# Kernel optimization log

Measured on AMD Instinct MI355X. Metric: run time of the kernel, lower is better.

## Reference

```python
import jax, jax.numpy as jnp
import numpy as np

D_MODEL = 1024
D_FF = 4096
NUM_EXPERTS = 8
TOP_K = 2


def setup_inputs() -> dict:
    key = jax.random.key(0)
    ks = jax.random.split(key, 9)
    s_in = 1.0 / np.sqrt(D_MODEL)
    s_ff = 1.0 / np.sqrt(D_FF)
    return {
        "x": jax.random.normal(ks[0], (2, 1024, D_MODEL), dtype=jnp.float32),
        "Wg": jax.random.uniform(ks[1], (D_MODEL, NUM_EXPERTS), minval=-s_in, maxval=s_in, dtype=jnp.float32),
        "bg": jax.random.uniform(ks[2], (NUM_EXPERTS,), minval=-s_in, maxval=s_in, dtype=jnp.float32),
        "W1": jax.random.uniform(ks[3], (NUM_EXPERTS, D_MODEL, D_FF), minval=-s_in, maxval=s_in, dtype=jnp.float32),
        "b1": jax.random.uniform(ks[4], (NUM_EXPERTS, D_FF), minval=-s_in, maxval=s_in, dtype=jnp.float32),
        "W2": jax.random.uniform(ks[5], (NUM_EXPERTS, D_MODEL, D_FF), minval=-s_in, maxval=s_in, dtype=jnp.float32),
        "b2": jax.random.uniform(ks[6], (NUM_EXPERTS, D_FF), minval=-s_in, maxval=s_in, dtype=jnp.float32),
        "W3": jax.random.uniform(ks[7], (NUM_EXPERTS, D_FF, D_MODEL), minval=-s_ff, maxval=s_ff, dtype=jnp.float32),
        "b3": jax.random.uniform(ks[8], (NUM_EXPERTS, D_MODEL), minval=-s_ff, maxval=s_ff, dtype=jnp.float32),
    }


def reference(x, Wg, bg, W1, b1, W2, b2, W3, b3):
    B, S, D = x.shape
    xf = x.reshape(-1, D)                                   # [N, D]
    N = xf.shape[0]

    # ---- Router (eval mode: no noise) ----
    logits = xf @ Wg + bg                                   # [N, E]
    top_logits, top_idx = jax.lax.top_k(logits, TOP_K)      # [N, K]
    top_w = jax.nn.softmax(top_logits, axis=-1)             # softmax over the top-k logits
    # scatter top-k weights into dense [N, E]; indices are unique per row
    comb_w = jnp.zeros_like(logits).at[jnp.arange(N)[:, None], top_idx].set(top_w)

    # ---- Experts: GLU-MLP, dense per-expert (weights are 0 for unrouted tokens) ----
    h1 = jnp.einsum('nd,edf->enf', xf, W1) + b1[:, None, :]  # [E, N, F]
    h2 = jnp.einsum('nd,edf->enf', xf, W2) + b2[:, None, :]
    hidden = jax.nn.gelu(h1, approximate=False) * h2         # torch nn.GELU is exact (erf)
    expert_out = jnp.einsum('enf,efd->end', hidden, W3) + b3[:, None, :]  # [E, N, D]

    # ---- Weighted combine ----
    final = jnp.einsum('end,ne->nd', expert_out, comb_w)     # [N, D]
    aux_loss = 0.0  # eval mode: aux loss inactive
    return final.reshape(B, S, D), aux_loss
```

## Files before the change

### kernel.cpp

```cpp
#include <hip/hip_runtime.h>
#include <hip/hip_bf16.h>
#include <math.h>

#define D_MODEL 1024
#define D_FF    4096
#define NE      8
#define MT      256

typedef __bf16 bf16x8 __attribute__((ext_vector_type(8)));
typedef float  f32x4  __attribute__((ext_vector_type(4)));

__device__ __forceinline__ void async16(const void* g, void* l) {
    __builtin_amdgcn_global_load_lds(
        (__attribute__((address_space(1))) uint32_t*)g,
        (__attribute__((address_space(3))) uint32_t*)l, 16, 0, 0);
}

__device__ __forceinline__ void transpose_tile_k128(
    const float* __restrict__ s, __bf16* __restrict__ d,
    int K, int N, int kt, int nt, int tid, float (*tile)[65])
{
    int tr = tid >> 4, tc = (tid & 15) * 4;
#pragma unroll
    for (int p = 0; p < 8; ++p) {
        float4 v = *reinterpret_cast<const float4*>(
            s + (size_t)(kt + tr + p * 16) * N + nt + tc);
        tile[tr + p * 16][tc + 0] = v.x;
        tile[tr + p * 16][tc + 1] = v.y;
        tile[tr + p * 16][tc + 2] = v.z;
        tile[tr + p * 16][tc + 3] = v.w;
    }
    __syncthreads();
    int kq = (tid & 15) * 8;
#pragma unroll
    for (int p = 0; p < 4; ++p) {
        int rr = (tid >> 4) + p * 16;
        bf16x8 pk;
#pragma unroll
        for (int i = 0; i < 8; ++i) pk[i] = (__bf16)tile[kq + i][rr];
        *reinterpret_cast<bf16x8*>(d + (size_t)(nt + rr) * K + kt + kq) = pk;
    }
}

__global__ __launch_bounds__(256) void fused_pre(
    const float* __restrict__ x, const float* __restrict__ Wg,
    const float* __restrict__ bg, int* __restrict__ topidx,
    float* __restrict__ topw, __bf16* __restrict__ Xb,
    const float* __restrict__ W1, const float* __restrict__ W2,
    const float* __restrict__ W3,
    __bf16* __restrict__ W1t, __bf16* __restrict__ W2t,
    __bf16* __restrict__ W3t, int nrouter)
{
    __shared__ float buf[128][65];
    int bid = blockIdx.x, tid = threadIdx.x;

    if (bid >= nrouter) {
        int tt = bid - nrouter;
        if (tt < 2 * 4096) {
            const float* s = W1; __bf16* d = W1t;
            if (tt >= 4096) { s = W2; d = W2t; tt -= 4096; }
            int e = tt >> 9, rem = tt & 511;
            int kt_i = rem >> 6, nt_i = rem & 63;
            transpose_tile_k128(s + ((size_t)e << 22), d + ((size_t)e << 22),
                                D_MODEL, D_FF, kt_i * 128, nt_i * 64, tid, buf);
        } else {
            tt -= 2 * 4096;
            int e = tt >> 9, rem = tt & 511;
            int kt_i = rem >> 4, nt_i = rem & 15;
            transpose_tile_k128(W3 + ((size_t)e << 22), W3t + ((size_t)e << 22),
                                D_FF, D_MODEL, kt_i * 128, nt_i * 64, tid, buf);
        }
        return;
    }

    int n = bid;
    const float* xr = x + (size_t)n * D_MODEL;
    int d0 = tid * 4;
    float4 xv = *reinterpret_cast<const float4*>(xr + d0);

    union { __bf16 h[4]; ushort4 u; } pk;
    pk.h[0] = (__bf16)xv.x; pk.h[1] = (__bf16)xv.y;
    pk.h[2] = (__bf16)xv.z; pk.h[3] = (__bf16)xv.w;
    *reinterpret_cast<ushort4*>(Xb + (size_t)n * D_MODEL + d0) = pk.u;

    float part[NE];
#pragma unroll
    for (int e = 0; e < NE; ++e) part[e] = 0.f;
    float xs[4] = {xv.x, xv.y, xv.z, xv.w};
#pragma unroll
    for (int j = 0; j < 4; ++j) {
        const float4* wr = reinterpret_cast<const float4*>(Wg + (size_t)(d0 + j) * NE);
        float4 w0 = wr[0], w1 = wr[1];
        part[0] += xs[j] * w0.x; part[1] += xs[j] * w0.y;
        part[2] += xs[j] * w0.z; part[3] += xs[j] * w0.w;
        part[4] += xs[j] * w1.x; part[5] += xs[j] * w1.y;
        part[6] += xs[j] * w1.z; part[7] += xs[j] * w1.w;
    }
#pragma unroll
    for (int off = 32; off > 0; off >>= 1) {
#pragma unroll
        for (int e = 0; e < NE; ++e) part[e] += __shfl_down(part[e], off);
    }
    float* sred = &buf[0][0];
    float* slog = &buf[1][0];
    int wave = tid >> 6, lane = tid & 63;
    if (lane == 0) {
#pragma unroll
        for (int e = 0; e < NE; ++e) sred[wave * NE + e] = part[e];
    }
    __syncthreads();
    if (tid < NE)
        slog[tid] = bg[tid] + sred[tid] + sred[NE + tid] + sred[2 * NE + tid] + sred[3 * NE + tid];
    __syncthreads();
    if (tid == 0) {
        float m0 = -1e30f, m1 = -1e30f; int i0 = 0, i1 = 0;
        for (int e = 0; e < NE; ++e) {
            float l = slog[e];
            if (l > m0)      { m1 = m0; i1 = i0; m0 = l; i0 = e; }
            else if (l > m1) { m1 = l;  i1 = e; }
        }
        float w1 = expf(m1 - m0);
        float s  = 1.f + w1;
        topidx[n * 2 + 0] = i0; topidx[n * 2 + 1] = i1;
        topw[n * 2 + 0] = 1.f / s; topw[n * 2 + 1] = w1 / s;
    }
}

__global__ __launch_bounds__(256) void build_lists_kernel(
    const int* __restrict__ topidx, const float* __restrict__ topw,
    int* __restrict__ pairTok, float* __restrict__ pairW,
    int* __restrict__ rbe, int* __restrict__ pairRow,
    int npairs, int maxrows, int maxblk)
{
    __shared__ int cnt[NE], cur[NE], pof[NE];
    int tid = threadIdx.x;
    if (tid < NE) { cnt[tid] = 0; cur[tid] = 0; }
    for (int i = tid; i < maxrows; i += 256) pairTok[i] = -1;
    for (int i = tid; i < maxblk; i += 256) rbe[i] = -1;
    __syncthreads();
    for (int p = tid; p < npairs; p += 256) atomicAdd(&cnt[topidx[p]], 1);
    __syncthreads();
    if (tid == 0) {
        int off = 0;
        for (int e = 0; e < NE; ++e) { pof[e] = off; off += (cnt[e] + MT - 1) & ~(MT - 1); }
        for (int e = 0; e < NE; ++e) {
            int nb = (cnt[e] + MT - 1) / MT;
            for (int j = 0; j < nb; ++j) rbe[pof[e] / MT + j] = e;
        }
    }
    __syncthreads();
    for (int p = tid; p < npairs; p += 256) {
        int e = topidx[p];
        int pos = atomicAdd(&cur[e], 1);
        int r = pof[e] + pos;
        pairTok[r]  = p >> 1;
        pairW[r]    = topw[p];
        pairRow[p]  = r;
    }
}

__global__ __launch_bounds__(512) void gemm1_mfma(
    const __bf16* __restrict__ Xb, const __bf16* __restrict__ W1t,
    const __bf16* __restrict__ W2t, const float* __restrict__ b1,
    const float* __restrict__ b2, const int* __restrict__ pairTok,
    const int* __restrict__ rbe, const __bf16* __restrict__ zpg,
    __bf16* __restrict__ hidden)
{
    int b = blockIdx.x;
    int e = rbe[b];
    if (e < 0) return;
    int fblk = blockIdx.y * 128;

    __shared__ __bf16 smem[2][32768];

    int tid = threadIdx.x, w = tid >> 6, l = tid & 63;
    int srcslot = (l & 7) ^ (l >> 3);
    int r0 = b * MT;

    const __bf16* aptr[4];
#pragma unroll
    for (int j = 0; j < 4; ++j) {
        int row = w * 32 + j * 8 + (l >> 3);
        int tok = pairTok[r0 + row];
        aptr[j] = (tok >= 0 ? Xb + (size_t)tok * D_MODEL : zpg) + srcslot * 8;
    }
    const __bf16* b1base = W1t + ((size_t)e << 22)
        + (size_t)(fblk + w * 16 + (l >> 3)) * D_MODEL + srcslot * 8;
    const __bf16* b2base = W2t + ((size_t)e << 22)
        + (size_t)(fblk + w * 16 + (l >> 3)) * D_MODEL + srcslot * 8;

    int wm = (w >> 1) * 64, wf = (w & 1) * 64;
    int lm = l & 15;

    f32x4 c1[4][4], c2[4][4];
#pragma unroll
    for (int mi = 0; mi < 4; ++mi)
#pragma unroll
        for (int fj = 0; fj < 4; ++fj) {
            c1[mi][fj] = (f32x4){0.f, 0.f, 0.f, 0.f};
            c2[mi][fj] = (f32x4){0.f, 0.f, 0.f, 0.f};
        }

    auto stage = [&](int buf, int k0) {
        __bf16* base = &smem[buf][0];
#pragma unroll
        for (int j = 0; j < 4; ++j)
            async16(aptr[j] + k0, base + w * 2048 + j * 512);
        async16(b1base + k0,               base + 16384 + w * 1024);
        async16(b1base + 8 * D_MODEL + k0, base + 16384 + w * 1024 + 512);
        async16(b2base + k0,               base + 24576 + w * 1024);
        async16(b2base + 8 * D_MODEL + k0, base + 24576 + w * 1024 + 512);
    };

    stage(0, 0);
    stage(1, 64);
    asm volatile("s_waitcnt vmcnt(8)" ::: "memory");
    __builtin_amdgcn_s_barrier();

    const int NT = D_MODEL / 64;
    for (int t = 0; t < NT; ++t) {
        int cur = t & 1;
        const __bf16* sb = &smem[cur][0];
#pragma unroll
        for (int ks = 0; ks < 2; ++ks) {
            int sl = (((ks * 4 + (l >> 4)) ^ (l & 7)) << 3);
            bf16x8 a[4], bv[4];
#pragma unroll
            for (int mi = 0; mi < 4; ++mi)
                a[mi] = *reinterpret_cast<const bf16x8*>(sb + (wm + mi * 16 + lm) * 64 + sl);
#pragma unroll
            for (int fj = 0; fj < 4; ++fj)
                bv[fj] = *reinterpret_cast<const bf16x8*>(sb + 16384 + (wf + fj * 16 + lm) * 64 + sl);
            __builtin_amdgcn_s_setprio(1);
#pragma unroll
            for (int fj = 0; fj < 4; ++fj)
#pragma unroll
                for (int mi = 0; mi < 4; ++mi)
                    c1[mi][fj] = __builtin_amdgcn_mfma_f32_16x16x32_bf16(a[mi], bv[fj], c1[mi][fj], 0, 0, 0);
            __builtin_amdgcn_s_setprio(0);
            __builtin_amdgcn_s_barrier();
#pragma unroll
            for (int fj = 0; fj < 4; ++fj)
                bv[fj] = *reinterpret_cast<const bf16x8*>(sb + 24576 + (wf + fj * 16 + lm) * 64 + sl);
            __builtin_amdgcn_s_setprio(1);
#pragma unroll
            for (int fj = 0; fj < 4; ++fj)
#pragma unroll
                for (int mi = 0; mi < 4; ++mi)
                    c2[mi][fj] = __builtin_amdgcn_mfma_f32_16x16x32_bf16(a[mi], bv[fj], c2[mi][fj], 0, 0, 0);
            __builtin_amdgcn_s_setprio(0);
            __builtin_amdgcn_s_barrier();
        }
        if (t + 2 < NT) {
            stage(cur, (t + 2) * 64);
            asm volatile("s_waitcnt vmcnt(8)" ::: "memory");
        } else if (t + 1 < NT) {
            asm volatile("s_waitcnt vmcnt(0)" ::: "memory");
        }
        __builtin_amdgcn_s_barrier();
    }

#pragma unroll
    for (int fj = 0; fj < 4; ++fj) {
        int f = fblk + wf + fj * 16 + lm;
        float b1v = b1[e * D_FF + f];
        float b2v = b2[e * D_FF + f];
#pragma unroll
        for (int mi = 0; mi < 4; ++mi)
#pragma unroll
            for (int r = 0; r < 4; ++r) {
                int m = wm + mi * 16 + (l >> 4) * 4 + r;
                float h1 = c1[mi][fj][r] + b1v;
                float h2 = c2[mi][fj][r] + b2v;
                float g = 0.5f * h1 * (1.f + erff(h1 * 0.70710678118654752f));
                hidden[(size_t)(r0 + m) * D_FF + f] = (__bf16)(g * h2);
            }
    }
}

__global__ __launch_bounds__(512, 4) void gemm2_mfma(
    const __bf16* __restrict__ hidden, const __bf16* __restrict__ W3t,
    const float* __restrict__ b3, const int* __restrict__ rbe,
    float* __restrict__ po)
{
    int rb = blockIdx.x;
    int e = rbe[rb >> 1];
    if (e < 0) return;
    int dblk = blockIdx.y * 128;

    __shared__ __bf16 smem[2][16384];

    int tid = threadIdx.x, w = tid >> 6, l = tid & 63;
    int ss8 = (l & 7) ^ (l >> 3);
    int r0m = rb * 128;

    const __bf16* abase = hidden + (size_t)(r0m + w * 16 + (l >> 3)) * D_FF + ss8 * 8;
    const __bf16* bbase = W3t + ((size_t)e << 22)
        + (size_t)(dblk + w * 16 + (l >> 3)) * D_FF + ss8 * 8;

    int wm = (w >> 1) * 32, wn = (w & 1) * 64;
    int lm = l & 15;

    f32x4 c[2][4];
#pragma unroll
    for (int mi = 0; mi < 2; ++mi)
#pragma unroll
        for (int nj = 0; nj < 4; ++nj) c[mi][nj] = (f32x4){0.f, 0.f, 0.f, 0.f};

    auto stage = [&](int buf, int k0) {
        __bf16* base = &smem[buf][0];
        async16(abase + k0,              base + w * 1024 + l * 8);
        async16(abase + 8 * D_FF + k0,   base + w * 1024 + 512 + l * 8);
        async16(bbase + k0,              base + 8192 + w * 1024 + l * 8);
        async16(bbase + 8 * D_FF + k0,   base + 8192 + w * 1024 + 512 + l * 8);
    };

    stage(0, 0);
    __syncthreads();
    const int NT = D_FF / 64;
    for (int t = 0; t < NT; ++t) {
        int cur = t & 1;
        if (t + 1 < NT) stage(cur ^ 1, (t + 1) * 64);
        const __bf16* sb = &smem[cur][0];
#pragma unroll
        for (int ks = 0; ks < 2; ++ks) {
            int sl = (((ks * 4 + (l >> 4)) ^ (l & 7)) << 3);
            bf16x8 a[2];
#pragma unroll
            for (int mi = 0; mi < 2; ++mi)
                a[mi] = *reinterpret_cast<const bf16x8*>(sb + (wm + mi * 16 + lm) * 64 + sl);
#pragma unroll
            for (int nj = 0; nj < 4; ++nj) {
                bf16x8 bv = *reinterpret_cast<const bf16x8*>(sb + 8192 + (wn + nj * 16 + lm) * 64 + sl);
#pragma unroll
                for (int mi = 0; mi < 2; ++mi)
                    c[mi][nj] = __builtin_amdgcn_mfma_f32_16x16x32_bf16(a[mi], bv, c[mi][nj], 0, 0, 0);
            }
        }
        __syncthreads();
    }

#pragma unroll
    for (int nj = 0; nj < 4; ++nj) {
        int d = dblk + wn + nj * 16 + lm;
        float b3v = b3[e * D_MODEL + d];
#pragma unroll
        for (int mi = 0; mi < 2; ++mi)
#pragma unroll
            for (int r = 0; r < 4; ++r) {
                int m = wm + mi * 16 + (l >> 4) * 4 + r;
                po[(size_t)(r0m + m) * D_MODEL + d] = c[mi][nj][r] + b3v;
            }
    }
}

__global__ __launch_bounds__(256) void combine_kernel(
    const float* __restrict__ po, const float* __restrict__ topw,
    const int* __restrict__ pairRow, float* __restrict__ out)
{
    int t = blockIdx.x, tid = threadIdx.x;
    int d = tid * 4;
    float w0 = topw[t * 2], w1 = topw[t * 2 + 1];
    int r0 = pairRow[t * 2], r1 = pairRow[t * 2 + 1];
    float4 v0 = *reinterpret_cast<const float4*>(po + (size_t)r0 * D_MODEL + d);
    float4 v1 = *reinterpret_cast<const float4*>(po + (size_t)r1 * D_MODEL + d);
    float4 o;
    o.x = w0 * v0.x + w1 * v1.x;
    o.y = w0 * v0.y + w1 * v1.y;
    o.z = w0 * v0.z + w1 * v1.z;
    o.w = w0 * v0.w + w1 * v1.w;
    *reinterpret_cast<float4*>(out + (size_t)t * D_MODEL + d) = o;
}

extern "C" void kernel_launch(void* const* d_in, const int* in_sizes, int n_in,
                              void* d_out, int out_size, void* d_ws, size_t ws_size,
                              hipStream_t stream)
{
    const float* x  = (const float*)d_in[0];
    const float* Wg = (const float*)d_in[1];
    const float* bg = (const float*)d_in[2];
    const float* W1 = (const float*)d_in[3];
    const float* b1 = (const float*)d_in[4];
    const float* W2 = (const float*)d_in[5];
    const float* b2 = (const float*)d_in[6];
    const float* W3 = (const float*)d_in[7];
    const float* b3 = (const float*)d_in[8];
    float* out = (float*)d_out;

    int N = in_sizes[0] / D_MODEL;
    int npairs = N * 2;
    int maxblk = npairs / MT + NE;
    int maxrows = maxblk * MT;

    char* ws = (char*)d_ws;
    size_t off = 0;
    auto alloc = [&](size_t bytes) -> void* {
        void* p = ws + off;
        off = (off + bytes + 255) & ~(size_t)255;
        return p;
    };
    int*    topidx  = (int*)   alloc((size_t)npairs * 4);
    float*  topw    = (float*) alloc((size_t)npairs * 4);
    int*    pairTok = (int*)   alloc((size_t)maxrows * 4);
    float*  pairW   = (float*) alloc((size_t)maxrows * 4);
    int*    rbe     = (int*)   alloc((size_t)maxblk * 4);
    int*    pairRow = (int*)   alloc((size_t)npairs * 4);
    __bf16* Xb      = (__bf16*)alloc((size_t)N * D_MODEL * 2);
    __bf16* hidden  = (__bf16*)alloc((size_t)maxrows * D_FF * 2);
    __bf16* zpg     = (__bf16*)alloc(4096);
    const size_t WSZ = (size_t)NE * D_MODEL * D_FF * 2;
    __bf16* W1t = (__bf16*)alloc(WSZ);
    __bf16* W2t = (__bf16*)alloc(WSZ);
    __bf16* W3t = (__bf16*)alloc(WSZ);
    float*  po  = (float*)W1t;
    (void)ws_size; (void)n_in; (void)pairW;

    hipMemsetAsync(zpg, 0, 4096, stream);

    fused_pre<<<N + 3 * 4096, 256, 0, stream>>>(
        x, Wg, bg, topidx, topw, Xb, W1, W2, W3, W1t, W2t, W3t, N);
    build_lists_kernel<<<1, 256, 0, stream>>>(topidx, topw, pairTok, pairW, rbe,
                                              pairRow, npairs, maxrows, maxblk);
    gemm1_mfma<<<dim3(maxblk, D_FF / 128), 512, 0, stream>>>(
        Xb, W1t, W2t, b1, b2, pairTok, rbe, zpg, hidden);
    gemm2_mfma<<<dim3(maxblk * 2, D_MODEL / 128), 512, 0, stream>>>(
        hidden, W3t, b3, rbe, po);
    combine_kernel<<<N, 256, 0, stream>>>(po, topw, pairRow, out);
}
```

Before: 342.3 us.

## Switch gemm1 to a 4-slot, K=32 async LDS pipeline with deeper prefetch

Restructures the gated GEMM1 main loop from double-buffered K=64 tiles to four ring buffers of K=32 tiles, prefetching three stages ahead and issuing the next stage's async loads right after the LDS fragment reads. The LDS swizzle and the per-lane global addressing are reworked for the 32-wide rows, and the vmcnt waits are retuned for the tail iterations. The aim is to hide global-load latency better and cut the number of barriers per K step. In exchange there are twice as many loop iterations, and the 4-way swizzle may introduce LDS bank conflicts.

```diff
diff --git a/kernel.cpp b/kernel.cpp
--- a/kernel.cpp
+++ b/kernel.cpp
@@ -171,26 +171,26 @@
     if (e < 0) return;
     int fblk = blockIdx.y * 128;
 
-    __shared__ __bf16 smem[2][32768];
+    __shared__ __bf16 smem[4][16384];
 
     int tid = threadIdx.x, w = tid >> 6, l = tid & 63;
-    int srcslot = (l & 7) ^ (l >> 3);
+    int ss4 = (l & 3) ^ ((l >> 3) & 3);
     int r0 = b * MT;
 
-    const __bf16* aptr[4];
-#pragma unroll
-    for (int j = 0; j < 4; ++j) {
-        int row = w * 32 + j * 8 + (l >> 3);
+    const __bf16* aptr[2];
+#pragma unroll
+    for (int j = 0; j < 2; ++j) {
+        int row = w * 32 + j * 16 + (l >> 2);
         int tok = pairTok[r0 + row];
-        aptr[j] = (tok >= 0 ? Xb + (size_t)tok * D_MODEL : zpg) + srcslot * 8;
-    }
-    const __bf16* b1base = W1t + ((size_t)e << 22)
-        + (size_t)(fblk + w * 16 + (l >> 3)) * D_MODEL + srcslot * 8;
-    const __bf16* b2base = W2t + ((size_t)e << 22)
-        + (size_t)(fblk + w * 16 + (l >> 3)) * D_MODEL + srcslot * 8;
+        aptr[j] = (tok >= 0 ? Xb + (size_t)tok * D_MODEL : zpg) + ss4 * 8;
+    }
+    int wrow = fblk + w * 16 + (l >> 2);
+    const __bf16* b1ptr = W1t + ((size_t)e << 22) + (size_t)wrow * D_MODEL + ss4 * 8;
+    const __bf16* b2ptr = W2t + ((size_t)e << 22) + (size_t)wrow * D_MODEL + ss4 * 8;
 
     int wm = (w >> 1) * 64, wf = (w & 1) * 64;
     int lm = l & 15;
+    int sl = (((l >> 4) ^ ((lm >> 1) & 3)) << 3);
 
     f32x4 c1[4][4], c2[4][4];
 #pragma unroll
@@ -201,62 +201,52 @@
             c2[mi][fj] = (f32x4){0.f, 0.f, 0.f, 0.f};
         }
 
-    auto stage = [&](int buf, int k0) {
-        __bf16* base = &smem[buf][0];
-#pragma unroll
-        for (int j = 0; j < 4; ++j)
-            async16(aptr[j] + k0, base + w * 2048 + j * 512);
-        async16(b1base + k0,               base + 16384 + w * 1024);
-        async16(b1base + 8 * D_MODEL + k0, base + 16384 + w * 1024 + 512);
-        async16(b2base + k0,               base + 24576 + w * 1024);
-        async16(b2base + 8 * D_MODEL + k0, base + 24576 + w * 1024 + 512);
+    auto stage = [&](int reg, int k0) {
+        __bf16* base = &smem[reg][0];
+        async16(aptr[0] + k0, base + w * 1024 + l * 8);
+        async16(aptr[1] + k0, base + w * 1024 + 512 + l * 8);
+        async16(b1ptr + k0, base + 8192 + w * 512 + l * 8);
+        async16(b2ptr + k0, base + 12288 + w * 512 + l * 8);
     };
 
+    const int NH = D_MODEL / 32;
     stage(0, 0);
-    stage(1, 64);
+    stage(1, 32);
+    stage(2, 64);
     asm volatile("s_waitcnt vmcnt(8)" ::: "memory");
     __builtin_amdgcn_s_barrier();
 
-    const int NT = D_MODEL / 64;
-    for (int t = 0; t < NT; ++t) {
-        int cur = t & 1;
-        const __bf16* sb = &smem[cur][0];
-#pragma unroll
-        for (int ks = 0; ks < 2; ++ks) {
-            int sl = (((ks * 4 + (l >> 4)) ^ (l & 7)) << 3);
-            bf16x8 a[4], bv[4];
+    for (int s = 0; s < NH; ++s) {
+        const __bf16* sb = &smem[s & 3][0];
+        bf16x8 a[4], bv[4];
+#pragma unroll
+        for (int mi = 0; mi < 4; ++mi)
+            a[mi] = *reinterpret_cast<const bf16x8*>(sb + (wm + mi * 16 + lm) * 32 + sl);
+#pragma unroll
+        for (int fj = 0; fj < 4; ++fj)
+            bv[fj] = *reinterpret_cast<const bf16x8*>(sb + 8192 + (wf + fj * 16 + lm) * 32 + sl);
+        if (s + 3 < NH) stage((s + 3) & 3, (s + 3) * 32);
+        __builtin_amdgcn_s_setprio(1);
+#pragma unroll
+        for (int fj = 0; fj < 4; ++fj)
 #pragma unroll
             for (int mi = 0; mi < 4; ++mi)
-                a[mi] = *reinterpret_cast<const bf16x8*>(sb + (wm + mi * 16 + lm) * 64 + sl);
-#pragma unroll
-            for (int fj = 0; fj < 4; ++fj)
-                bv[fj] = *reinterpret_cast<const bf16x8*>(sb + 16384 + (wf + fj * 16 + lm) * 64 + sl);
-            __builtin_amdgcn_s_setprio(1);
-#pragma unroll
-            for (int fj = 0; fj < 4; ++fj)
-#pragma unroll
-                for (int mi = 0; mi < 4; ++mi)
-                    c1[mi][fj] = __builtin_amdgcn_mfma_f32_16x16x32_bf16(a[mi], bv[fj], c1[mi][fj], 0, 0, 0);
-            __builtin_amdgcn_s_setprio(0);
-            __builtin_amdgcn_s_barrier();
-#pragma unroll
-            for (int fj = 0; fj < 4; ++fj)
-                bv[fj] = *reinterpret_cast<const bf16x8*>(sb + 24576 + (wf + fj * 16 + lm) * 64 + sl);
-            __builtin_amdgcn_s_setprio(1);
-#pragma unroll
-            for (int fj = 0; fj < 4; ++fj)
-#pragma unroll
-                for (int mi = 0; mi < 4; ++mi)
-                    c2[mi][fj] = __builtin_amdgcn_mfma_f32_16x16x32_bf16(a[mi], bv[fj], c2[mi][fj], 0, 0, 0);
-            __builtin_amdgcn_s_setprio(0);
-            __builtin_amdgcn_s_barrier();
-        }
-        if (t + 2 < NT) {
-            stage(cur, (t + 2) * 64);
-            asm volatile("s_waitcnt vmcnt(8)" ::: "memory");
-        } else if (t + 1 < NT) {
-            asm volatile("s_waitcnt vmcnt(0)" ::: "memory");
-        }
+                c1[mi][fj] = __builtin_amdgcn_mfma_f32_16x16x32_bf16(a[mi], bv[fj], c1[mi][fj], 0, 0, 0);
+        __builtin_amdgcn_s_setprio(0);
+        __builtin_amdgcn_s_barrier();
+#pragma unroll
+        for (int fj = 0; fj < 4; ++fj)
+            bv[fj] = *reinterpret_cast<const bf16x8*>(sb + 12288 + (wf + fj * 16 + lm) * 32 + sl);
+        __builtin_amdgcn_s_setprio(1);
+#pragma unroll
+        for (int fj = 0; fj < 4; ++fj)
+#pragma unroll
+            for (int mi = 0; mi < 4; ++mi)
+                c2[mi][fj] = __builtin_amdgcn_mfma_f32_16x16x32_bf16(a[mi], bv[fj], c2[mi][fj], 0, 0, 0);
+        __builtin_amdgcn_s_setprio(0);
+        if (s + 3 < NH)      asm volatile("s_waitcnt vmcnt(8)" ::: "memory");
+        else if (s + 2 < NH) asm volatile("s_waitcnt vmcnt(4)" ::: "memory");
+        else if (s + 1 < NH) asm volatile("s_waitcnt vmcnt(0)" ::: "memory");
         __builtin_amdgcn_s_barrier();
     }
 
```

Result: no change. 349.0 us (+1.9%).
